# Performance work log

Hardware: AMD Instinct MI355X
Metric: run time of the kernel (lower is better)

## Reference

```python
import jax, jax.numpy as jnp
import numpy as np

R = 7        # rcnn_crop_size[cls_ind]
SCALE = 4    # cfg['stride']


def _pool1d(x, c0, c1, K):
    # Adaptive max pool along leading axis of x ([F, ...] -> [R, ...]).
    # torch AdaptiveMaxPool bins: start_i = floor(i*L/R), end_i = ceil((i+1)*L/R)
    F = x.shape[0]
    L = c1 - c0
    i = jnp.arange(R)
    starts = c0 + (i * L) // R
    ends = c0 + ((i + 1) * L + R - 1) // R
    idx = starts[:, None] + jnp.arange(K)[None, :]           # [R, K], K bounds max bin length
    g = x[jnp.clip(idx, 0, F - 1)]                           # [R, K, ...]
    valid = (idx < ends[:, None]).reshape((R, K) + (1,) * (x.ndim - 1))
    return jnp.max(jnp.where(valid, g, jnp.finfo(x.dtype).min), axis=1)


def _crop_pool(f, dims_max, p, Ks):
    # One proposal: variable-size crop from f[b] + adaptive max pool to [C,R,R,R].
    b = p[0].astype(jnp.int32)
    center, side = p[2:5], p[5:8]
    c0 = jnp.floor((center - side / 2) / SCALE).astype(jnp.int32)
    c1 = jnp.ceil((center + side / 2) / SCALE).astype(jnp.int32)
    c0 = jnp.maximum(c0, 0)
    c1 = jnp.minimum(c1, dims_max)
    x = f[b]                                                 # [C, Fd, Fh, Fw]
    for ax in range(3):                                      # separable adaptive max pool
        x = jnp.moveaxis(x, ax + 1, 0)
        x = _pool1d(x, c0[ax], c1[ax], Ks[ax])
        x = jnp.moveaxis(x, 0, ax + 1)
    return x                                                 # [C, R, R, R]


def setup_inputs() -> dict:
    key = jax.random.key(0)
    kf, kb, ks, kc, kd = jax.random.split(key, 5)
    B, C, Fs = 4, 64, 32
    N = 96
    f = jax.random.normal(kf, (B, C, Fs, Fs, Fs), dtype=jnp.float32)
    inputs = jnp.zeros((B, 1, 128, 128, 128), dtype=jnp.float32)
    bidx = jax.random.randint(kb, (N, 1), 0, B).astype(jnp.float32)
    score = jax.random.uniform(ks, (N, 1), dtype=jnp.float32)
    centers = jax.random.uniform(kc, (N, 3), minval=24.0, maxval=104.0, dtype=jnp.float32)
    sides = jax.random.uniform(kd, (N, 3), minval=8.0, maxval=48.0, dtype=jnp.float32)
    proposals = jnp.concatenate([bidx, score, centers, sides], axis=1)  # [N, 8]
    return {"f": f, "inputs": inputs, "proposals": proposals, "cls_ind": 0}


def reference(f, inputs, proposals, cls_ind):
    D, H, W = inputs.shape[2], inputs.shape[3], inputs.shape[4]
    dims_max = jnp.array([D // SCALE, H // SCALE, W // SCALE], dtype=jnp.int32)
    # max bin length per axis for any crop length L <= F: ceil(F/R)+1
    Ks = tuple(-(-f.shape[ax + 2] // R) + 1 for ax in range(3))
    return jax.vmap(lambda p: _crop_pool(f, dims_max, p, Ks))(proposals)  # [N, C, R, R, R]
```

## Files before the change

kernel.cpp:

```cpp
#include <hip/hip_runtime.h>
#include <float.h>


#define NTHREADS 256
#define NCH 4
#define MAXL 13
#define MAXV (MAXL * MAXL * MAXL)
#define BATCH 9

__global__ __launch_bounds__(NTHREADS, 4) void crop_roi_v8(
        const float* __restrict__ f,
        const float* __restrict__ props,
        float* __restrict__ out,
        int C) {
    __shared__ float4 s4[MAXV];
    const int cbase = blockIdx.x * NCH;
    const int n = blockIdx.y;
    const int tid = threadIdx.x;

    const float* p = props + (size_t)n * 8;
    const int b = (int)p[0];

    int d0 = (int)floorf((p[2] - p[5] * 0.5f) * 0.25f);
    int d1 = (int)ceilf ((p[2] + p[5] * 0.5f) * 0.25f);
    int h0 = (int)floorf((p[3] - p[6] * 0.5f) * 0.25f);
    int h1 = (int)ceilf ((p[3] + p[6] * 0.5f) * 0.25f);
    int w0 = (int)floorf((p[4] - p[7] * 0.5f) * 0.25f);
    int w1 = (int)ceilf ((p[4] + p[7] * 0.5f) * 0.25f);
    d0 = max(d0, 0); d1 = min(d1, 32);
    h0 = max(h0, 0); h1 = min(h1, 32);
    w0 = max(w0, 0); w1 = min(w1, 32);
    const int Ld = d1 - d0, Lh = h1 - h0, Lw = w1 - w0;

    const float* base0 = f + (((size_t)b * C + cbase) << 15);
    const int nch = min(NCH, C - cbase);

    size_t choff[NCH];
#pragma unroll
    for (int cs = 0; cs < NCH; ++cs)
        choff[cs] = (size_t)min(cs, nch - 1) << 15;

    if (Ld >= 1 && Ld <= MAXL && Lh >= 1 && Lh <= MAXL && Lw >= 1 && Lw <= MAXL) {
        const int D1 = Lh * Lw;
        const int V  = Ld * D1;
        const unsigned Mdh = (D1 > 1) ? (unsigned)(0x100000000ULL / (unsigned)D1) + 1u : 0u;
        const unsigned Mw  = (Lw > 1) ? (unsigned)(0x100000000ULL / (unsigned)Lw) + 1u : 0u;

        float rv[BATCH][NCH];
        int   ec[BATCH];
#pragma unroll
        for (int u = 0; u < BATCH; ++u) {
            const int e = tid + u * NTHREADS;
            if (e < V) {
                unsigned d = (D1 > 1) ? __umulhi((unsigned)e, Mdh) : (unsigned)e;
                unsigned r = (unsigned)e - d * (unsigned)D1;
                unsigned h = (Lw > 1) ? __umulhi(r, Mw) : r;
                unsigned w = r - h * (unsigned)Lw;
                const int g = ((((d0 + (int)d) << 5) + (h0 + (int)h)) << 5)
                              + w0 + (int)w;
                ec[u] = e;
#pragma unroll
                for (int cs = 0; cs < NCH; ++cs)
                    rv[u][cs] = base0[choff[cs] + g];
            }
        }
#pragma unroll
        for (int u = 0; u < BATCH; ++u) {
            if (tid + u * NTHREADS < V) {
                s4[ec[u]] = make_float4(rv[u][0], rv[u][1], rv[u][2], rv[u][3]);
            }
        }
        __syncthreads();

        for (int o = tid; o < 343; o += NTHREADS) {
            const int i = o / 49;
            const int j = (o / 7) % 7;
            const int k = o % 7;
            const int a0 = (i * Ld) / 7,  a1 = ((i + 1) * Ld + 6) / 7;
            const int b0 = (j * Lh) / 7,  b1 = ((j + 1) * Lh + 6) / 7;
            const int g0 = (k * Lw) / 7,  g1 = ((k + 1) * Lw + 6) / 7;
            const int dd[3] = { a0, min(a0 + 1, a1 - 1), a1 - 1 };
            const int hh[3] = { b0, min(b0 + 1, b1 - 1), b1 - 1 };
            const int ww[3] = { g0, min(g0 + 1, g1 - 1), g1 - 1 };
            float m0 = -FLT_MAX, m1 = -FLT_MAX, m2 = -FLT_MAX, m3 = -FLT_MAX;
#pragma unroll
            for (int x = 0; x < 3; ++x) {
#pragma unroll
                for (int y = 0; y < 3; ++y) {
                    const int rowb = (dd[x] * Lh + hh[y]) * Lw;
#pragma unroll
                    for (int z = 0; z < 3; ++z) {
                        const float4 v = s4[rowb + ww[z]];
                        m0 = fmaxf(m0, v.x);
                        m1 = fmaxf(m1, v.y);
                        m2 = fmaxf(m2, v.z);
                        m3 = fmaxf(m3, v.w);
                    }
                }
            }
            const float mm[NCH] = { m0, m1, m2, m3 };
            for (int cs = 0; cs < nch; ++cs)
                out[((size_t)n * C + cbase + cs) * 343 + o] = mm[cs];
        }
    } else {
        for (int o = tid; o < 343; o += NTHREADS) {
            const int i = o / 49, j = (o / 7) % 7, k = o % 7;
            const int ds = d0 + (i * Ld) / 7, de = d0 + ((i + 1) * Ld + 6) / 7;
            const int hs = h0 + (j * Lh) / 7, he = h0 + ((j + 1) * Lh + 6) / 7;
            const int ws = w0 + (k * Lw) / 7, we = w0 + ((k + 1) * Lw + 6) / 7;
            for (int cs = 0; cs < nch; ++cs) {
                float m = -FLT_MAX;
                const float* basec = base0 + ((size_t)cs << 15);
                for (int d = ds; d < de; ++d)
                    for (int h = hs; h < he; ++h) {
                        const float* row = basec + (d << 10) + (h << 5);
                        for (int w = ws; w < we; ++w) m = fmaxf(m, row[w]);
                    }
                out[((size_t)n * C + cbase + cs) * 343 + o] = m;
            }
        }
    }
}

extern "C" void kernel_launch(void* const* d_in, const int* in_sizes, int n_in,
                              void* d_out, int out_size, void* d_ws, size_t ws_size,
                              hipStream_t stream) {
    const float* f = (const float*)d_in[0];
    const float* props = (const float*)d_in[2];

    int N = in_sizes[2] / 8;
    int C = out_size / (N * 343);

    dim3 block(NTHREADS);
    dim3 grid((C + NCH - 1) / NCH, N);
    crop_roi_v8<<<grid, block, 0, stream>>>(f, props, (float*)d_out, C);
}
```

Baseline: 100.7 us.

## Pre-reduce the W axis during global load to shrink shared tile

The kernel now performs the W-axis adaptive max while loading from global memory. Each thread reads the three candidate W elements for an output column and stores one reduced value per (d,h,k) into a smaller shared buffer of Ld*Lh*7 entries. The second stage then does only nine shared reads per output instead of 27. Block size rises to 384 so that one thread handles each of the 343 outputs, and the occupancy hint is dropped. Global loads become redundant and less coalesced because neighbouring k bins re-read overlapping W elements.

New measurement: 103.2 us. 2.5% more time.

```diff
diff --git a/kernel.cpp b/kernel.cpp
--- a/kernel.cpp
+++ b/kernel.cpp
@@ -2,18 +2,18 @@
 #include <float.h>
 
 
-#define NTHREADS 256
+#define NTHREADS 384
 #define NCH 4
 #define MAXL 13
-#define MAXV (MAXL * MAXL * MAXL)
-#define BATCH 9
+#define MAXT (MAXL * MAXL * 7)
+#define BATCH 4
 
-__global__ __launch_bounds__(NTHREADS, 4) void crop_roi_v8(
+__global__ __launch_bounds__(NTHREADS) void crop_roi_v9(
         const float* __restrict__ f,
         const float* __restrict__ props,
         float* __restrict__ out,
         int C) {
-    __shared__ float4 s4[MAXV];
+    __shared__ float4 t1[MAXT];
     const int cbase = blockIdx.x * NCH;
     const int n = blockIdx.y;
     const int tid = threadIdx.x;
@@ -41,61 +41,54 @@
         choff[cs] = (size_t)min(cs, nch - 1) << 15;
 
     if (Ld >= 1 && Ld <= MAXL && Lh >= 1 && Lh <= MAXL && Lw >= 1 && Lw <= MAXL) {
-        const int D1 = Lh * Lw;
-        const int V  = Ld * D1;
-        const unsigned Mdh = (D1 > 1) ? (unsigned)(0x100000000ULL / (unsigned)D1) + 1u : 0u;
-        const unsigned Mw  = (Lw > 1) ? (unsigned)(0x100000000ULL / (unsigned)Lw) + 1u : 0u;
+        const int Vt = Ld * Lh * 7;
+        const unsigned Mh = (Lh > 1) ? (unsigned)(0x100000000ULL / (unsigned)Lh) + 1u : 0u;
 
-        float rv[BATCH][NCH];
-        int   ec[BATCH];
 #pragma unroll
         for (int u = 0; u < BATCH; ++u) {
             const int e = tid + u * NTHREADS;
-            if (e < V) {
-                unsigned d = (D1 > 1) ? __umulhi((unsigned)e, Mdh) : (unsigned)e;
-                unsigned r = (unsigned)e - d * (unsigned)D1;
-                unsigned h = (Lw > 1) ? __umulhi(r, Mw) : r;
-                unsigned w = r - h * (unsigned)Lw;
-                const int g = ((((d0 + (int)d) << 5) + (h0 + (int)h)) << 5)
-                              + w0 + (int)w;
-                ec[u] = e;
+            if (e < Vt) {
+                const int k = e % 7;
+                const int q = e / 7;
+                const int h = (Lh > 1) ? (q - (int)__umulhi((unsigned)q, Mh) * Lh) : 0;
+                const int d = (Lh > 1) ? (int)__umulhi((unsigned)q, Mh) : q;
+                const int g0 = (k * Lw) / 7;
+                const int g1 = ((k + 1) * Lw + 6) / 7;
+                const int wA = g0, wB = min(g0 + 1, g1 - 1), wC = g1 - 1;
+                const int gb = ((((d0 + d) << 5) + (h0 + h)) << 5) + w0;
+                float mx[NCH];
 #pragma unroll
-                for (int cs = 0; cs < NCH; ++cs)
-                    rv[u][cs] = base0[choff[cs] + g];
-            }
-        }
-#pragma unroll
-        for (int u = 0; u < BATCH; ++u) {
-            if (tid + u * NTHREADS < V) {
-                s4[ec[u]] = make_float4(rv[u][0], rv[u][1], rv[u][2], rv[u][3]);
+                for (int cs = 0; cs < NCH; ++cs) {
+                    const float* bc = base0 + choff[cs] + gb;
+                    const float vA = bc[wA];
+                    const float vB = bc[wB];
+                    const float vC = bc[wC];
+                    mx[cs] = fmaxf(fmaxf(vA, vB), vC);
+                }
+                t1[e] = make_float4(mx[0], mx[1], mx[2], mx[3]);
             }
         }
         __syncthreads();
 
-        for (int o = tid; o < 343; o += NTHREADS) {
+        if (tid < 343) {
+            const int o = tid;
             const int i = o / 49;
             const int j = (o / 7) % 7;
             const int k = o % 7;
             const int a0 = (i * Ld) / 7,  a1 = ((i + 1) * Ld + 6) / 7;
             const int b0 = (j * Lh) / 7,  b1 = ((j + 1) * Lh + 6) / 7;
-            const int g0 = (k * Lw) / 7,  g1 = ((k + 1) * Lw + 6) / 7;
             const int dd[3] = { a0, min(a0 + 1, a1 - 1), a1 - 1 };
             const int hh[3] = { b0, min(b0 + 1, b1 - 1), b1 - 1 };
-            const int ww[3] = { g0, min(g0 + 1, g1 - 1), g1 - 1 };
             float m0 = -FLT_MAX, m1 = -FLT_MAX, m2 = -FLT_MAX, m3 = -FLT_MAX;
 #pragma unroll
             for (int x = 0; x < 3; ++x) {
 #pragma unroll
                 for (int y = 0; y < 3; ++y) {
-                    const int rowb = (dd[x] * Lh + hh[y]) * Lw;
-#pragma unroll
-                    for (int z = 0; z < 3; ++z) {
-                        const float4 v = s4[rowb + ww[z]];
-                        m0 = fmaxf(m0, v.x);
-                        m1 = fmaxf(m1, v.y);
-                        m2 = fmaxf(m2, v.z);
-                        m3 = fmaxf(m3, v.w);
-                    }
+                    const float4 v = t1[(dd[x] * Lh + hh[y]) * 7 + k];
+                    m0 = fmaxf(m0, v.x);
+                    m1 = fmaxf(m1, v.y);
+                    m2 = fmaxf(m2, v.z);
+                    m3 = fmaxf(m3, v.w);
                 }
             }
             const float mm[NCH] = { m0, m1, m2, m3 };
@@ -133,5 +126,5 @@
 
     dim3 block(NTHREADS);
     dim3 grid((C + NCH - 1) / NCH, N);
-    crop_roi_v8<<<grid, block, 0, stream>>>(f, props, (float*)d_out, C);
+    crop_roi_v9<<<grid, block, 0, stream>>>(f, props, (float*)d_out, C);
 }
```
